# Kernel tuning notes

Hardware: AMD Instinct MI355X
Metric: run time of the kernel (lower is better)

Reference implementation:

```python
import jax, jax.numpy as jnp
import numpy as np

DIST_THRESH = 0.1
W_DIST = 0.05
W_CHAMFER = 0.05
W_SEP = 0.0005


def setup_inputs() -> dict:
    key = jax.random.key(0)
    k1, k2, k3, k4 = jax.random.split(key, 4)
    B, N, K = 4, 200000, 64
    return {
        "landmarks_C": jax.random.uniform(k1, (B, N, 3), jnp.float32),          # predicted point coords
        "landmarks_F": jax.random.normal(k2, (B, N, 4), jnp.float32) * 0.05,    # [dist, dx, dy, dz]
        "targets_C": jax.random.uniform(k3, (B, K, 3), jnp.float32),            # GT landmark coords
        "targets_F": jax.random.randint(k4, (B, K), 0, 8),                      # GT landmark class labels
        "classes": jnp.arange(6),                                               # classes to supervise
    }


def reference(landmarks_C, landmarks_F, targets_C, targets_F, classes):
    def per_batch(C_i, F_i, tC, tF):
        # class mask over GT landmarks (replaces boolean indexing in torch)
        mask_k = jnp.any(tF[None, :] == classes[:, None], axis=0)          # [K]
        n_valid = mask_k.sum()
        dists_i = F_i[:, 0]                                                # predicted distance, [N]
        coords_i = C_i + F_i[:, 1:]                                        # refined coords, [N,3]
        # pairwise dists GT landmarks -> raw point coords, invalid classes pushed to +inf
        pd = jnp.linalg.norm(C_i[None, :, :] - tC[:, None, :], axis=-1)    # [K,N]
        pd = jnp.where(mask_k[:, None], pd, jnp.inf)
        min_d = pd.min(axis=0)                                             # [N]
        pm = min_d < DIST_THRESH                                           # points near some GT landmark
        # smooth-L1 (beta=1, sum) on predicted distance; clip(inf)=2*thresh reproduces empty-target fallback
        tgt = jnp.clip(min_d, 0.0, 2.0 * DIST_THRESH)
        diff = dists_i - tgt
        ad = jnp.abs(diff)
        dist_loss = jnp.where(ad < 1.0, 0.5 * diff * diff, ad - 0.5).sum()
        # pairwise dists GT landmarks -> refined coords
        ld = jnp.linalg.norm(coords_i[None, :, :] - tC[:, None, :], axis=-1)  # [K,N]
        ld_m = jnp.where(mask_k[:, None], ld, jnp.inf)
        p2g = jnp.where(pm, ld_m.min(axis=0), 0.0)                         # pred->gt, masked points only
        g2p = jnp.where(mask_k, ld_m.min(axis=1), 0.0)                     # gt->pred, valid GT only
        chamfer = (p2g * p2g).sum() + (g2p * g2p).sum()
        # separation: ratio of dists to 2 nearest (valid) GT landmarks, per masked point
        _, idx = jax.lax.top_k(-pd.T, 2)                                   # [N,2] indices of 2 smallest
        d01 = jnp.take_along_axis(ld.T, idx, axis=1)                       # [N,2]
        sep = jnp.where(pm, d01[:, 0] / d01[:, 1], 0.0).sum()
        sep = jnp.where(n_valid >= 2, sep, 0.0)
        return W_DIST * dist_loss + W_CHAMFER * chamfer + W_SEP * sep

    losses = jax.vmap(per_batch)(landmarks_C, landmarks_F, targets_C, targets_F)
    return losses.mean()
```

## Files before the change

### kernel.cpp

```cpp
#include <hip/hip_runtime.h>


constexpr int KT = 64;
constexpr int P  = 8;
constexpr int NREP = 16;
constexpr float DIST_THRESH = 0.1f;
constexpr float W_DIST    = 0.05f;
constexpr float W_CHAMFER = 0.05f;
constexpr float W_SEP     = 0.0005f;
constexpr float PT_SENT = -1e18f;
constexpr float TG_SENT = -1e18f;
constexpr float BIGF  = 3.0e38f;
constexpr float WBIAS = 16.0f;

typedef float f2 __attribute__((ext_vector_type(2)));

__device__ __forceinline__ unsigned umin_(unsigned a, unsigned b) { return a < b ? a : b; }
__device__ __forceinline__ unsigned umax_(unsigned a, unsigned b) { return a > b ? a : b; }

__device__ __forceinline__ f2 pk_fma(f2 a, f2 b, f2 c) {
#if __has_builtin(__builtin_elementwise_fma)
    return __builtin_elementwise_fma(a, b, c);
#else
    f2 r; r.x = fmaf(a.x, b.x, c.x); r.y = fmaf(a.y, b.y, c.y); return r;
#endif
}

__global__ __launch_bounds__(128, 3)
void landmark_main(const float* __restrict__ C, const float* __restrict__ F,
                   const float* __restrict__ tC, const int* __restrict__ tF,
                   const int* __restrict__ classes, int n_classes, int N,
                   unsigned int* __restrict__ g2p_rep, float* __restrict__ sums_rep)
{
    __shared__ float4   tgtFull[KT];
    __shared__ unsigned g2pLDS[KT];
    __shared__ uint4    mK1a[64], mK1b[64];
    __shared__ uint4    mK2a[64], mK2b[64];
    __shared__ float4   mLMa[64], mLMb[64];

    const int tid   = threadIdx.x;
    const int lane  = tid & 63;
    const int h     = tid >> 6;
    const int l31   = lane & 31;
    const int hi5   = lane >> 5;
    const int blk   = blockIdx.x;
    const int b     = blk & 3;
    const int chunk = blk >> 2;
    const int rep   = chunk & (NREP - 1);

    if (tid < KT) {
        int f = tF[b * KT + tid];
        bool valid = false;
        for (int c = 0; c < n_classes; ++c) valid = valid || (f == classes[c]);
        float x = TG_SENT, y = TG_SENT, z = TG_SENT;
        if (valid) {
            x = tC[(b * KT + tid) * 3 + 0];
            y = tC[(b * KT + tid) * 3 + 1];
            z = tC[(b * KT + tid) * 3 + 2];
        }
        tgtFull[tid] = make_float4(-2.f * x, -2.f * y, -2.f * z,
                                   x * x + y * y + z * z + WBIAS);
        g2pLDS[tid] = 0x7F7FFFFFu;
    }
    __syncthreads();

    const float*  Cb = C + (size_t)b * N * 3;
    const float4* Fb = (const float4*)(F + (size_t)b * N * 4);
    const int base = chunk * (64 * P);

    f2 pcx[P], pcy[P], pcz[P];
    float ppm[P], ccm[P], f0[P];
    #pragma unroll
    for (int p = 0; p < P; ++p) {
        int n = base + p * 64 + lane;
        bool v = (n < N);
        int ni = v ? n : 0;
        float4 f4 = Fb[ni];
        float X = Cb[3 * ni + 0], Y = Cb[3 * ni + 1], Z = Cb[3 * ni + 2];
        f0[p] = v ? f4.x : 2.0f * DIST_THRESH;
        if (!v) { X = PT_SENT; Y = PT_SENT; Z = PT_SENT; f4.y = f4.z = f4.w = 0.f; }
        float cxv = X + f4.y, cyv = Y + f4.z, czv = Z + f4.w;
        pcx[p] = (f2){X, cxv};
        pcy[p] = (f2){Y, cyv};
        pcz[p] = (f2){Z, czv};
        ppm[p] = fmaf(Z, Z, fmaf(Y, Y, X * X)) - WBIAS;
        ccm[p] = fmaf(czv, czv, fmaf(cyv, cyv, cxv * cxv)) - WBIAS;
    }

    unsigned k1[P], k2[P];
    float lmin[P];
    #pragma unroll
    for (int p = 0; p < P; ++p) { k1[p] = 0xFFFFFFFFu; k2[p] = 0xFFFFFFFFu; lmin[p] = BIGF; }

    const unsigned tkb = (unsigned)((l31 ^ (hi5 << 4)) | (h << 5));
    #pragma unroll 4
    for (int i = 0; i < 32; ++i) {
        const unsigned tk = tkb ^ (unsigned)i;
        const float4 T = tgtFull[tk];
        const f2 Tx = {T.x, T.x}, Ty = {T.y, T.y}, Tz = {T.z, T.z}, Tw = {T.w, T.w};
        float av[P];
        #pragma unroll
        for (int p = 0; p < P; ++p) {
            f2 w2 = pk_fma(pcx[p], Tx, pk_fma(pcy[p], Ty, pk_fma(pcz[p], Tz, Tw)));
            unsigned key = (__float_as_uint(w2.x) & 0xFFFFFFC0u) | tk;
            unsigned hi = umax_(k1[p], key);
            k1[p] = umin_(k1[p], key);
            k2[p] = umin_(k2[p], hi);
            lmin[p] = fminf(lmin[p], w2.y);
            av[p] = w2.y + ccm[p];
        }
        float m01 = fminf(av[0], av[1]), m23 = fminf(av[2], av[3]);
        float m45 = fminf(av[4], av[5]), m67 = fminf(av[6], av[7]);
        float dl = fmaxf(fminf(fminf(m01, m23), fminf(m45, m67)), 0.f);
        atomicMin(&g2pLDS[tk], __float_as_uint(dl));
    }

    if (h == 0) {
        mK1a[lane] = make_uint4(k1[0], k1[1], k1[2], k1[3]);
        mK1b[lane] = make_uint4(k1[4], k1[5], k1[6], k1[7]);
        mK2a[lane] = make_uint4(k2[0], k2[1], k2[2], k2[3]);
        mK2b[lane] = make_uint4(k2[4], k2[5], k2[6], k2[7]);
        mLMa[lane] = make_float4(lmin[0], lmin[1], lmin[2], lmin[3]);
        mLMb[lane] = make_float4(lmin[4], lmin[5], lmin[6], lmin[7]);
    }
    __syncthreads();

    if (h == 0) {
        atomicMax(&g2p_rep[rep * 256 + b * 64 + lane], ~g2pLDS[lane]);
    } else {
        uint4 A1a = mK1a[lane], A1b = mK1b[lane];
        uint4 A2a = mK2a[lane], A2b = mK2b[lane];
        float4 ALa = mLMa[lane], ALb = mLMb[lane];
        const unsigned a1v[P] = {A1a.x, A1a.y, A1a.z, A1a.w, A1b.x, A1b.y, A1b.z, A1b.w};
        const unsigned a2v[P] = {A2a.x, A2a.y, A2a.z, A2a.w, A2b.x, A2b.y, A2b.z, A2b.w};
        const float    alv[P] = {ALa.x, ALa.y, ALa.z, ALa.w, ALb.x, ALb.y, ALb.z, ALb.w};

        float dist_acc = 0.f, p2g_acc = 0.f, sep_acc = 0.f;
        #pragma unroll
        for (int p = 0; p < P; ++p) {
            unsigned m1 = umin_(a1v[p], k1[p]);
            unsigned m2 = umin_(umax_(a1v[p], k1[p]), umin_(a2v[p], k2[p]));
            float lm = fminf(alv[p], lmin[p]);
            float keyf1 = __uint_as_float(m1 & 0xFFFFFFC0u);
            float mind = sqrtf(fmaxf(keyf1 + ppm[p], 0.f));
            bool pm = mind < DIST_THRESH;
            float tgtv = fminf(mind, 2.0f * DIST_THRESH);
            float diff = f0[p] - tgtv;
            float ad = fabsf(diff);
            dist_acc += (ad < 1.0f) ? 0.5f * diff * diff : (ad - 0.5f);
            if (pm) {
                p2g_acc += fmaxf(lm + ccm[p], 0.f);
                int i1 = (int)(m1 & 63u), i2 = (int)(m2 & 63u);
                float4 T1 = tgtFull[i1], T2 = tgtFull[i2];
                float cxv = pcx[p].y, cyv = pcy[p].y, czv = pcz[p].y;
                float l1sq = fmaf(cxv, T1.x, fmaf(cyv, T1.y, fmaf(czv, T1.z, T1.w))) + ccm[p];
                float l2sq = fmaf(cxv, T2.x, fmaf(cyv, T2.y, fmaf(czv, T2.z, T2.w))) + ccm[p];
                sep_acc += sqrtf(fmaxf(l1sq, 0.f) / fmaxf(l2sq, 1e-30f));
            }
        }

        float v0 = dist_acc, v1 = p2g_acc, v2 = sep_acc;
        #pragma unroll
        for (int o = 32; o > 0; o >>= 1) {
            v0 += __shfl_down(v0, o, 64);
            v1 += __shfl_down(v1, o, 64);
            v2 += __shfl_down(v2, o, 64);
        }
        if (lane == 0) {
            float* sb = sums_rep + rep * 16 + b;
            atomicAdd(sb + 0, v0);
            atomicAdd(sb + 4, v1);
            atomicAdd(sb + 8, v2);
        }
    }
}

__global__ void landmark_finalize(const int* __restrict__ tF, const int* __restrict__ classes,
                                  int n_classes, const unsigned int* __restrict__ g2p_rep,
                                  const float* __restrict__ sums_rep, float* __restrict__ out)
{
    __shared__ float lossb[4];
    const int tid = threadIdx.x;
    const int b = tid >> 6, k = tid & 63;

    int f = tF[b * KT + k];
    bool valid = false;
    for (int c = 0; c < n_classes; ++c) valid = valid || (f == classes[c]);

    unsigned enc = 0;
    for (int r = 0; r < NREP; ++r) enc = umax_(enc, g2p_rep[r * 256 + b * 64 + k]);
    float g  = valid ? __uint_as_float(~enc) : 0.f;
    float nv = valid ? 1.f : 0.f;

    #pragma unroll
    for (int o = 32; o > 0; o >>= 1) {
        g  += __shfl_down(g, o, 64);
        nv += __shfl_down(nv, o, 64);
    }
    if (k == 0) {
        float sd = 0.f, sp = 0.f, ss = 0.f;
        for (int r = 0; r < NREP; ++r) {
            sd += sums_rep[r * 16 + 0 + b];
            sp += sums_rep[r * 16 + 4 + b];
            ss += sums_rep[r * 16 + 8 + b];
        }
        float sep = (nv >= 2.f) ? ss : 0.f;
        lossb[b] = W_DIST * sd + W_CHAMFER * (sp + g) + W_SEP * sep;
    }
    __syncthreads();
    if (tid == 0)
        out[0] = (lossb[0] + lossb[1] + lossb[2] + lossb[3]) * 0.25f;
}

extern "C" void kernel_launch(void* const* d_in, const int* in_sizes, int n_in,
                              void* d_out, int out_size, void* d_ws, size_t ws_size,
                              hipStream_t stream)
{
    const float* C       = (const float*)d_in[0];
    const float* F       = (const float*)d_in[1];
    const float* tC      = (const float*)d_in[2];
    const int*   tF      = (const int*)d_in[3];
    const int*   classes = (const int*)d_in[4];
    const int n_classes = in_sizes[4];
    const int B = 4;
    const int N = in_sizes[0] / (3 * B);

    unsigned int* g2p_rep  = (unsigned int*)d_ws;
    float*        sums_rep = (float*)((char*)d_ws + NREP * 256 * 4);

    hipMemsetAsync(d_ws, 0, NREP * 256 * 4 + NREP * 16 * 4, stream);

    const int cpb = (N + 64 * P - 1) / (64 * P);
    landmark_main<<<cpb * 4, 128, 0, stream>>>(C, F, tC, tF, classes, n_classes,
                                               N, g2p_rep, sums_rep);
    landmark_finalize<<<1, 256, 0, stream>>>(tF, classes, n_classes, g2p_rep,
                                             sums_rep, (float*)d_out);
}
```

Baseline: 103.6 us.

## Split each block into two half-chunks with prefetch of the second during compute

Each block still covers 512 points, but now as two sub-chunks of 256 points, with P reduced from 8 to 4 registers per lane. Loads for the second sub-chunk are issued before the first sub-chunk's target loop runs, so global-memory latency can hide behind compute. Launch bounds are raised to 4 waves to allow higher occupancy from the smaller register footprint. The cost is an extra pair of block barriers and twice as many LDS atomics and merge steps per point set.

Result: no change. 101.6 us (-1.9%).

```diff
diff --git a/kernel.cpp b/kernel.cpp
--- a/kernel.cpp
+++ b/kernel.cpp
@@ -2,7 +2,7 @@
 
 
 constexpr int KT = 64;
-constexpr int P  = 8;
+constexpr int P  = 4;
 constexpr int NREP = 16;
 constexpr float DIST_THRESH = 0.1f;
 constexpr float W_DIST    = 0.05f;
@@ -26,7 +26,7 @@
 #endif
 }
 
-__global__ __launch_bounds__(128, 3)
+__global__ __launch_bounds__(128, 4)
 void landmark_main(const float* __restrict__ C, const float* __restrict__ F,
                    const float* __restrict__ tC, const int* __restrict__ tF,
                    const int* __restrict__ classes, int n_classes, int N,
@@ -34,9 +34,8 @@
 {
     __shared__ float4   tgtFull[KT];
     __shared__ unsigned g2pLDS[KT];
-    __shared__ uint4    mK1a[64], mK1b[64];
-    __shared__ uint4    mK2a[64], mK2b[64];
-    __shared__ float4   mLMa[64], mLMb[64];
+    __shared__ uint4    mK1[64], mK2[64];
+    __shared__ float4   mLM[64];
 
     const int tid   = threadIdx.x;
     const int lane  = tid & 63;
@@ -45,8 +44,8 @@
     const int hi5   = lane >> 5;
     const int blk   = blockIdx.x;
     const int b     = blk & 3;
-    const int chunk = blk >> 2;
-    const int rep   = chunk & (NREP - 1);
+    const int pair  = blk >> 2;
+    const int rep   = pair & (NREP - 1);
 
     if (tid < KT) {
         int f = tF[b * KT + tid];
@@ -66,99 +65,120 @@
 
     const float*  Cb = C + (size_t)b * N * 3;
     const float4* Fb = (const float4*)(F + (size_t)b * N * 4);
-    const int base = chunk * (64 * P);
-
+    const int base0 = pair * 512;
+    const int base1 = base0 + 256;
+
+    float4 rf[P]; float rX[P], rY[P], rZ[P];
     f2 pcx[P], pcy[P], pcz[P];
     float ppm[P], ccm[P], f0[P];
-    #pragma unroll
-    for (int p = 0; p < P; ++p) {
-        int n = base + p * 64 + lane;
-        bool v = (n < N);
-        int ni = v ? n : 0;
-        float4 f4 = Fb[ni];
-        float X = Cb[3 * ni + 0], Y = Cb[3 * ni + 1], Z = Cb[3 * ni + 2];
-        f0[p] = v ? f4.x : 2.0f * DIST_THRESH;
-        if (!v) { X = PT_SENT; Y = PT_SENT; Z = PT_SENT; f4.y = f4.z = f4.w = 0.f; }
-        float cxv = X + f4.y, cyv = Y + f4.z, czv = Z + f4.w;
-        pcx[p] = (f2){X, cxv};
-        pcy[p] = (f2){Y, cyv};
-        pcz[p] = (f2){Z, czv};
-        ppm[p] = fmaf(Z, Z, fmaf(Y, Y, X * X)) - WBIAS;
-        ccm[p] = fmaf(czv, czv, fmaf(cyv, cyv, cxv * cxv)) - WBIAS;
-    }
-
     unsigned k1[P], k2[P];
     float lmin[P];
-    #pragma unroll
-    for (int p = 0; p < P; ++p) { k1[p] = 0xFFFFFFFFu; k2[p] = 0xFFFFFFFFu; lmin[p] = BIGF; }
+    float dist_acc = 0.f, p2g_acc = 0.f, sep_acc = 0.f;
+
+    auto issue_loads = [&](int baseN) {
+        #pragma unroll
+        for (int p = 0; p < P; ++p) {
+            int n = baseN + p * 64 + lane;
+            int ni = (n < N) ? n : 0;
+            rf[p] = Fb[ni];
+            rX[p] = Cb[3 * ni + 0];
+            rY[p] = Cb[3 * ni + 1];
+            rZ[p] = Cb[3 * ni + 2];
+        }
+    };
+    auto process = [&](int baseN) {
+        #pragma unroll
+        for (int p = 0; p < P; ++p) {
+            int n = baseN + p * 64 + lane;
+            bool v = (n < N);
+            float4 f4 = rf[p];
+            float X = rX[p], Y = rY[p], Z = rZ[p];
+            f0[p] = v ? f4.x : 2.0f * DIST_THRESH;
+            if (!v) { X = PT_SENT; Y = PT_SENT; Z = PT_SENT; f4.y = f4.z = f4.w = 0.f; }
+            float cxv = X + f4.y, cyv = Y + f4.z, czv = Z + f4.w;
+            pcx[p] = (f2){X, cxv};
+            pcy[p] = (f2){Y, cyv};
+            pcz[p] = (f2){Z, czv};
+            ppm[p] = fmaf(Z, Z, fmaf(Y, Y, X * X)) - WBIAS;
+            ccm[p] = fmaf(czv, czv, fmaf(cyv, cyv, cxv * cxv)) - WBIAS;
+        }
+    };
 
     const unsigned tkb = (unsigned)((l31 ^ (hi5 << 4)) | (h << 5));
-    #pragma unroll 4
-    for (int i = 0; i < 32; ++i) {
-        const unsigned tk = tkb ^ (unsigned)i;
-        const float4 T = tgtFull[tk];
-        const f2 Tx = {T.x, T.x}, Ty = {T.y, T.y}, Tz = {T.z, T.z}, Tw = {T.w, T.w};
-        float av[P];
-        #pragma unroll
-        for (int p = 0; p < P; ++p) {
-            f2 w2 = pk_fma(pcx[p], Tx, pk_fma(pcy[p], Ty, pk_fma(pcz[p], Tz, Tw)));
-            unsigned key = (__float_as_uint(w2.x) & 0xFFFFFFC0u) | tk;
-            unsigned hi = umax_(k1[p], key);
-            k1[p] = umin_(k1[p], key);
-            k2[p] = umin_(k2[p], hi);
-            lmin[p] = fminf(lmin[p], w2.y);
-            av[p] = w2.y + ccm[p];
-        }
-        float m01 = fminf(av[0], av[1]), m23 = fminf(av[2], av[3]);
-        float m45 = fminf(av[4], av[5]), m67 = fminf(av[6], av[7]);
-        float dl = fmaxf(fminf(fminf(m01, m23), fminf(m45, m67)), 0.f);
-        atomicMin(&g2pLDS[tk], __float_as_uint(dl));
-    }
-
-    if (h == 0) {
-        mK1a[lane] = make_uint4(k1[0], k1[1], k1[2], k1[3]);
-        mK1b[lane] = make_uint4(k1[4], k1[5], k1[6], k1[7]);
-        mK2a[lane] = make_uint4(k2[0], k2[1], k2[2], k2[3]);
-        mK2b[lane] = make_uint4(k2[4], k2[5], k2[6], k2[7]);
-        mLMa[lane] = make_float4(lmin[0], lmin[1], lmin[2], lmin[3]);
-        mLMb[lane] = make_float4(lmin[4], lmin[5], lmin[6], lmin[7]);
-    }
-    __syncthreads();
+
+    auto do_chunk = [&]() {
+        #pragma unroll
+        for (int p = 0; p < P; ++p) { k1[p] = 0xFFFFFFFFu; k2[p] = 0xFFFFFFFFu; lmin[p] = BIGF; }
+
+        #pragma unroll 8
+        for (int i = 0; i < 32; ++i) {
+            const unsigned tk = tkb ^ (unsigned)i;
+            const float4 T = tgtFull[tk];
+            const f2 Tx = {T.x, T.x}, Ty = {T.y, T.y}, Tz = {T.z, T.z}, Tw = {T.w, T.w};
+            float av[P];
+            #pragma unroll
+            for (int p = 0; p < P; ++p) {
+                f2 w2 = pk_fma(pcx[p], Tx, pk_fma(pcy[p], Ty, pk_fma(pcz[p], Tz, Tw)));
+                unsigned key = (__float_as_uint(w2.x) & 0xFFFFFFC0u) | tk;
+                unsigned hi = umax_(k1[p], key);
+                k1[p] = umin_(k1[p], key);
+                k2[p] = umin_(k2[p], hi);
+                lmin[p] = fminf(lmin[p], w2.y);
+                av[p] = w2.y + ccm[p];
+            }
+            float dl = fmaxf(fminf(fminf(av[0], av[1]), fminf(av[2], av[3])), 0.f);
+            atomicMin(&g2pLDS[tk], __float_as_uint(dl));
+        }
+
+        if (h == 0) {
+            mK1[lane] = make_uint4(k1[0], k1[1], k1[2], k1[3]);
+            mK2[lane] = make_uint4(k2[0], k2[1], k2[2], k2[3]);
+            mLM[lane] = make_float4(lmin[0], lmin[1], lmin[2], lmin[3]);
+        }
+        __syncthreads();
+
+        if (h == 1) {
+            uint4 A1 = mK1[lane], A2 = mK2[lane];
+            float4 AL = mLM[lane];
+            const unsigned a1v[P] = {A1.x, A1.y, A1.z, A1.w};
+            const unsigned a2v[P] = {A2.x, A2.y, A2.z, A2.w};
+            const float    alv[P] = {AL.x, AL.y, AL.z, AL.w};
+            #pragma unroll
+            for (int p = 0; p < P; ++p) {
+                unsigned m1 = umin_(a1v[p], k1[p]);
+                unsigned m2 = umin_(umax_(a1v[p], k1[p]), umin_(a2v[p], k2[p]));
+                float lm = fminf(alv[p], lmin[p]);
+                float keyf1 = __uint_as_float(m1 & 0xFFFFFFC0u);
+                float mind = sqrtf(fmaxf(keyf1 + ppm[p], 0.f));
+                bool pm = mind < DIST_THRESH;
+                float tgtv = fminf(mind, 2.0f * DIST_THRESH);
+                float diff = f0[p] - tgtv;
+                float ad = fabsf(diff);
+                dist_acc += (ad < 1.0f) ? 0.5f * diff * diff : (ad - 0.5f);
+                if (pm) {
+                    p2g_acc += fmaxf(lm + ccm[p], 0.f);
+                    int i1 = (int)(m1 & 63u), i2 = (int)(m2 & 63u);
+                    float4 T1 = tgtFull[i1], T2 = tgtFull[i2];
+                    float cxv = pcx[p].y, cyv = pcy[p].y, czv = pcz[p].y;
+                    float l1sq = fmaf(cxv, T1.x, fmaf(cyv, T1.y, fmaf(czv, T1.z, T1.w))) + ccm[p];
+                    float l2sq = fmaf(cxv, T2.x, fmaf(cyv, T2.y, fmaf(czv, T2.z, T2.w))) + ccm[p];
+                    sep_acc += sqrtf(fmaxf(l1sq, 0.f) / fmaxf(l2sq, 1e-30f));
+                }
+            }
+        }
+        __syncthreads();
+    };
+
+    issue_loads(base0);
+    process(base0);
+    issue_loads(base1);
+    do_chunk();
+    process(base1);
+    do_chunk();
 
     if (h == 0) {
         atomicMax(&g2p_rep[rep * 256 + b * 64 + lane], ~g2pLDS[lane]);
     } else {
-        uint4 A1a = mK1a[lane], A1b = mK1b[lane];
-        uint4 A2a = mK2a[lane], A2b = mK2b[lane];
-        float4 ALa = mLMa[lane], ALb = mLMb[lane];
-        const unsigned a1v[P] = {A1a.x, A1a.y, A1a.z, A1a.w, A1b.x, A1b.y, A1b.z, A1b.w};
-        const unsigned a2v[P] = {A2a.x, A2a.y, A2a.z, A2a.w, A2b.x, A2b.y, A2b.z, A2b.w};
-        const float    alv[P] = {ALa.x, ALa.y, ALa.z, ALa.w, ALb.x, ALb.y, ALb.z, ALb.w};
-
-        float dist_acc = 0.f, p2g_acc = 0.f, sep_acc = 0.f;
-        #pragma unroll
-        for (int p = 0; p < P; ++p) {
-            unsigned m1 = umin_(a1v[p], k1[p]);
-            unsigned m2 = umin_(umax_(a1v[p], k1[p]), umin_(a2v[p], k2[p]));
-            float lm = fminf(alv[p], lmin[p]);
-            float keyf1 = __uint_as_float(m1 & 0xFFFFFFC0u);
-            float mind = sqrtf(fmaxf(keyf1 + ppm[p], 0.f));
-            bool pm = mind < DIST_THRESH;
-            float tgtv = fminf(mind, 2.0f * DIST_THRESH);
-            float diff = f0[p] - tgtv;
-            float ad = fabsf(diff);
-            dist_acc += (ad < 1.0f) ? 0.5f * diff * diff : (ad - 0.5f);
-            if (pm) {
-                p2g_acc += fmaxf(lm + ccm[p], 0.f);
-                int i1 = (int)(m1 & 63u), i2 = (int)(m2 & 63u);
-                float4 T1 = tgtFull[i1], T2 = tgtFull[i2];
-                float cxv = pcx[p].y, cyv = pcy[p].y, czv = pcz[p].y;
-                float l1sq = fmaf(cxv, T1.x, fmaf(cyv, T1.y, fmaf(czv, T1.z, T1.w))) + ccm[p];
-                float l2sq = fmaf(cxv, T2.x, fmaf(cyv, T2.y, fmaf(czv, T2.z, T2.w))) + ccm[p];
-                sep_acc += sqrtf(fmaxf(l1sq, 0.f) / fmaxf(l2sq, 1e-30f));
-            }
-        }
-
         float v0 = dist_acc, v1 = p2g_acc, v2 = sep_acc;
         #pragma unroll
         for (int o = 32; o > 0; o >>= 1) {
@@ -230,9 +250,9 @@
 
     hipMemsetAsync(d_ws, 0, NREP * 256 * 4 + NREP * 16 * 4, stream);
 
-    const int cpb = (N + 64 * P - 1) / (64 * P);
-    landmark_main<<<cpb * 4, 128, 0, stream>>>(C, F, tC, tF, classes, n_classes,
-                                               N, g2p_rep, sums_rep);
+    const int pairs = (N + 511) / 512;
+    landmark_main<<<pairs * 4, 128, 0, stream>>>(C, F, tC, tF, classes, n_classes,
+                                                 N, g2p_rep, sums_rep);
     landmark_finalize<<<1, 256, 0, stream>>>(tF, classes, n_classes, g2p_rep,
                                              sums_rep, (float*)d_out);
 }
```
